# Performance work log

Hardware: AMD Instinct MI355X
Metric: run time of the kernel (lower is better)

## Reference

```python
import jax, jax.numpy as jnp
import numpy as np


def setup_inputs() -> dict:
    key = jax.random.key(0)
    x = jax.random.normal(key, (32, 64, 64, 64), dtype=jnp.float32)
    return {"x": x, "num_zeros": 2}


def reference(x, num_zeros):
    # ZeroWeave: interleave `num_zeros` zeros between every pair of pixels
    # along both spatial dims (equivalent to the gather_nd over
    # concat([x, zeros_like(x)]) with the precomputed index tensor).
    # x: [B, C, H, W] -> [B, C, H*s - num_zeros, W*s - num_zeros], s = num_zeros + 1
    s = num_zeros + 1
    B, C, H, W = x.shape
    out_h = H * s - num_zeros
    out_w = W * s - num_zeros
    out = jnp.zeros((B, C, out_h, out_w), dtype=x.dtype)
    out = out.at[:, :, ::s, ::s].set(x)
    return out
```

## Files before the change

### kernel.cpp

```cpp
#include <hip/hip_runtime.h>


constexpr int S  = 3;
constexpr int H  = 64;
constexpr int W  = 64;
constexpr int OH = H * S - (S - 1);
constexpr int OW = W * S - (S - 1);
constexpr int PLANE_IN = H * W;
constexpr int ROW2 = OW / 2;
constexpr long long N_OUT = 32LL * 64 * OH * OW;
constexpr int N2 = (int)(N_OUT / 2);
constexpr int BLOCK = 256;
constexpr int GRID = N2 / BLOCK;
static_assert(GRID * BLOCK == N2, "grid must cover output exactly");
static_assert(OW % 2 == 0, "row must be whole float2s");

__global__ __launch_bounds__(BLOCK) void ZeroWeave_89601607729830_kernel(
    const float* __restrict__ x, float* __restrict__ out) {
    int i = blockIdx.x * BLOCK + threadIdx.x;

    int row = i / ROW2;
    int j   = i - row * ROW2;
    int bc  = row / OH;
    int h   = row - bc * OH;

    float2 v = make_float2(0.0f, 0.0f);
    if (h % S == 0) {
        int w0 = 2 * j;
        int m  = w0 % S;
        const float* xr = x + bc * PLANE_IN + (h / S) * W;
        if (m == 0)      v.x = xr[w0 / S];
        else if (m == 2) v.y = xr[(w0 + 1) / S];
    }

    reinterpret_cast<float2*>(out)[i] = v;
}

extern "C" void kernel_launch(void* const* d_in, const int* in_sizes, int n_in,
                              void* d_out, int out_size, void* d_ws, size_t ws_size,
                              hipStream_t stream) {
    const float* x = (const float*)d_in[0];
    float* out = (float*)d_out;

    ZeroWeave_89601607729830_kernel<<<GRID, BLOCK, 0, stream>>>(x, out);
}
```

Measured before the change: 355.6 us.

## Assign one block per plane and split data rows from zero-only rows

Each block now handles one whole output plane and loops over it, instead of one thread per float2 across the whole tensor. Rows that carry input data are written by a loop that selects values branch-free, and the zero-only rows are written by a separate loop that stores constant zeros. Divisions are replaced by multiply-shift tricks. This removes per-element divide/modulo and branching on the zero rows, but the grid drops to 2048 blocks with long serial loops per thread, which may reduce memory-level parallelism.

```diff
diff --git a/kernel.cpp b/kernel.cpp
--- a/kernel.cpp
+++ b/kernel.cpp
@@ -1,39 +1,58 @@
 #include <hip/hip_runtime.h>
 
 
-constexpr int S  = 3;
-constexpr int H  = 64;
-constexpr int W  = 64;
-constexpr int OH = H * S - (S - 1);
-constexpr int OW = W * S - (S - 1);
-constexpr int PLANE_IN = H * W;
-constexpr int ROW2 = OW / 2;
-constexpr long long N_OUT = 32LL * 64 * OH * OW;
-constexpr int N2 = (int)(N_OUT / 2);
-constexpr int BLOCK = 256;
-constexpr int GRID = N2 / BLOCK;
-static_assert(GRID * BLOCK == N2, "grid must cover output exactly");
-static_assert(OW % 2 == 0, "row must be whole float2s");
+constexpr int PLANE_IN  = 64 * 64;
+constexpr int PLANE_F2  = 190 * 190 / 2;
+constexpr int NPLANES   = 32 * 64;
+constexpr int BLOCK     = 256;
+
+constexpr int NC = 64 * 95;
+constexpr int C_FULL = NC / BLOCK;
+constexpr int C_TAIL = NC - C_FULL * BLOCK;
+
+constexpr int NZ = 63 * 190;
+constexpr int Z_FULL = NZ / BLOCK;
+constexpr int Z_TAIL = NZ - Z_FULL * BLOCK;
 
 __global__ __launch_bounds__(BLOCK) void ZeroWeave_89601607729830_kernel(
     const float* __restrict__ x, float* __restrict__ out) {
-    int i = blockIdx.x * BLOCK + threadIdx.x;
+    const int bc = blockIdx.x;
+    const int t  = threadIdx.x;
 
-    int row = i / ROW2;
-    int j   = i - row * ROW2;
-    int bc  = row / OH;
-    int h   = row - bc * OH;
+    const float* xp = x + bc * PLANE_IN;
+    float2* o2 = reinterpret_cast<float2*>(out) + bc * PLANE_F2;
 
-    float2 v = make_float2(0.0f, 0.0f);
-    if (h % S == 0) {
-        int w0 = 2 * j;
-        int m  = w0 % S;
-        const float* xr = x + bc * PLANE_IN + (h / S) * W;
-        if (m == 0)      v.x = xr[w0 / S];
-        else if (m == 2) v.y = xr[(w0 + 1) / S];
-    }
+    auto compose = [&](int idx) {
+        unsigned u  = (unsigned)idx;
+        unsigned r  = (u * 5519u) >> 19;
+        unsigned j  = u - r * 95u;
+        unsigned a  = (j * 171u) >> 9;
+        unsigned jm = j - a * 3u;
+        unsigned w3 = 2u * a + (jm == 1u);
+        float val = xp[(r << 6) + w3];
+        float2 v;
+        v.x = (jm == 0u) ? val : 0.0f;
+        v.y = (jm == 1u) ? val : 0.0f;
+        o2[285u * r + j] = v;
+    };
+#pragma unroll 4
+    for (int k = 0; k < C_FULL; ++k)
+        compose(k * BLOCK + t);
+    if (t < C_TAIL)
+        compose(C_FULL * BLOCK + t);
 
-    reinterpret_cast<float2*>(out)[i] = v;
+    const float2 z2 = make_float2(0.0f, 0.0f);
+    auto zero = [&](int idx) {
+        unsigned u = (unsigned)idx;
+        unsigned s = (u * 5519u) >> 20;
+        unsigned j = u - s * 190u;
+        o2[285u * s + 95u + j] = z2;
+    };
+#pragma unroll 8
+    for (int k = 0; k < Z_FULL; ++k)
+        zero(k * BLOCK + t);
+    if (t < Z_TAIL)
+        zero(Z_FULL * BLOCK + t);
 }
 
 extern "C" void kernel_launch(void* const* d_in, const int* in_sizes, int n_in,
@@ -42,5 +61,5 @@
     const float* x = (const float*)d_in[0];
     float* out = (float*)d_out;
 
-    ZeroWeave_89601607729830_kernel<<<GRID, BLOCK, 0, stream>>>(x, out);
+    ZeroWeave_89601607729830_kernel<<<NPLANES, BLOCK, 0, stream>>>(x, out);
 }
```

New measurement: 372.2 us. 4.7% more time.
